# Optimization experiments

Measured on AMD Instinct MI355X. Metric: run time of the kernel, lower is better.

Reference implementation:

```python
import jax, jax.numpy as jnp
import numpy as np

N = 50000
NEG_SLOPE = 0.2


def add_self_loops(edge_index, n):
    loop = jnp.arange(n, dtype=edge_index.dtype)
    return jnp.concatenate([edge_index, jnp.stack([loop, loop])], axis=1)


def gatv2_conv(x, edge_index, Wl, bl, Wr, br, att, bias):
    """PyG GATv2Conv (share_weights=False, concat=True, add_self_loops applied by caller).
    x: [N, Fin]; edge_index: [2, E] with row0=src(j), row1=dst(i); att: [H, D].
    Returns (out [N, H*D], alpha [E, H])."""
    src, dst = edge_index[0], edge_index[1]
    H, D = att.shape
    n = x.shape[0]
    xl = (x @ Wl + bl).reshape(n, H, D)   # source-side transform
    xr = (x @ Wr + br).reshape(n, H, D)   # target-side transform
    e = jax.nn.leaky_relu(xl[src] + xr[dst], NEG_SLOPE)        # [E, H, D]
    logit = jnp.einsum('ehd,hd->eh', e, att)                    # [E, H]
    # segment softmax over edges grouped by target node
    lmax = jax.ops.segment_max(logit, dst, num_segments=n)      # [N, H]
    ex = jnp.exp(logit - lmax[dst])
    denom = jax.ops.segment_sum(ex, dst, num_segments=n)
    alpha = ex / denom[dst]                                     # [E, H]
    out = jax.ops.segment_sum(alpha[:, :, None] * xl[src], dst, num_segments=n)  # [N, H, D]
    return out.reshape(n, H * D) + bias, alpha


def setup_inputs() -> dict:
    key = jax.random.key(0)
    ks = jax.random.split(key, 16)
    E = 400000
    x = jax.random.normal(ks[0], (N, 23), dtype=jnp.float32)
    edge_index = jax.random.randint(ks[1], (2, E), 0, N, dtype=jnp.int64)
    H1, D1 = 8, 64
    F1 = H1 * D1  # 512
    s = 0.1
    return {
        'x': x,
        'edge_index': edge_index,
        'Wl1': jax.random.normal(ks[2], (23, F1), dtype=jnp.float32) * s,
        'bl1': jnp.zeros((F1,), jnp.float32),
        'Wr1': jax.random.normal(ks[3], (23, F1), dtype=jnp.float32) * s,
        'br1': jnp.zeros((F1,), jnp.float32),
        'att1': jax.random.normal(ks[4], (H1, D1), dtype=jnp.float32) * s,
        'bias1': jnp.zeros((F1,), jnp.float32),
        'Wl2': jax.random.normal(ks[5], (F1, 1), dtype=jnp.float32) * s,
        'bl2': jnp.zeros((1,), jnp.float32),
        'Wr2': jax.random.normal(ks[6], (F1, 1), dtype=jnp.float32) * s,
        'br2': jnp.zeros((1,), jnp.float32),
        'att2': jax.random.normal(ks[7], (1, 1), dtype=jnp.float32) * s,
        'bias2': jnp.zeros((1,), jnp.float32),
    }


def reference(x, edge_index, Wl1, bl1, Wr1, br1, att1, bias1,
              Wl2, bl2, Wr2, br2, att2, bias2):
    ei = add_self_loops(edge_index, N)
    h, _ = gatv2_conv(x, ei, Wl1, bl1, Wr1, br1, att1, bias1)
    h = jax.nn.relu(h)
    h, alpha = gatv2_conv(h, ei, Wl2, bl2, Wr2, br2, att2, bias2)
    return h, alpha
```

## Files before the change

### kernel.cpp

```cpp
#include <hip/hip_runtime.h>
#include <math.h>

#define NN 50000
#define E0 400000
#define EE 450000
#define FF 512
#define G1 2048
#define NPB 25
#define EPB 220
#define WAVES_TOTAL (G1 * 4)
#define MAXD 64
#define LOG2E 1.44269504f

typedef _Float16 h2 __attribute__((ext_vector_type(2)));

__device__ __forceinline__ h2 uas_h2(unsigned u) { union { unsigned u; h2 h; } c; c.u = u; return c.h; }
__device__ __forceinline__ unsigned h2as_u(h2 h) { union { unsigned u; h2 h; } c; c.h = h; return c.u; }
__device__ __forceinline__ unsigned packh(float a, float b) {
    h2 hh = { (_Float16)a, (_Float16)b };
    return h2as_u(hh);
}
__device__ __forceinline__ float leaky(float v) { return fmaxf(v, 0.2f * v); }

template <int CTRL>
__device__ __forceinline__ float dpp_add(float v) {
    int x = __builtin_bit_cast(int, v);
    int y = __builtin_amdgcn_update_dpp(0, x, CTRL, 0xF, 0xF, true);
    return v + __builtin_bit_cast(float, y);
}

__global__ __launch_bounds__(256) void k_predeg(
    const float* __restrict__ x,
    const float* __restrict__ Wl1, const float* __restrict__ bl1,
    const float* __restrict__ Wr1, const float* __restrict__ br1,
    const int* __restrict__ ei,
    unsigned* __restrict__ xlh, unsigned* __restrict__ xrh,
    int* __restrict__ cnt, int* __restrict__ src_sl)
{
    __shared__ unsigned sxh[NPB * 12];
    int b = blockIdx.x, t = threadIdx.x;

    {
        int e0 = b * EPB;
        int e1 = e0 + EPB; if (e1 > EE) e1 = EE;
        for (int e = e0 + t; e < e1; e += 256) {
            int src, dst;
            if (e < E0) { src = ei[e]; dst = ei[E0 + e]; }
            else        { src = e - E0; dst = src; }
            int p = atomicAdd(&cnt[dst], 1);
            if (p < MAXD) src_sl[(size_t)dst * MAXD + p] = src;
        }
    }

    int i0 = b * NPB;
    int i1 = i0 + NPB; if (i1 > NN) i1 = NN;
    int nnod = i1 - i0;
    for (int k = t; k < nnod * 12; k += 256) {
        int n = k / 12, j = k - n * 12;
        const float* row = x + (size_t)(i0 + n) * 23;
        float f0 = row[2 * j];
        float f1 = (2 * j + 1 < 23) ? row[2 * j + 1] : 0.f;
        sxh[n * 12 + j] = packh(f0, f1);
    }

    int c0 = 2 * t, c1 = 2 * t + 1;
    h2 wl0[12], wl1v[12], wr0[12], wr1v[12];
#pragma unroll
    for (int j = 0; j < 12; j++) {
        int r0 = 2 * j, r1 = 2 * j + 1;
        float a, b2;
        a = Wl1[r0 * FF + c0]; b2 = (r1 < 23) ? Wl1[r1 * FF + c0] : 0.f;
        wl0[j] = (h2){ (_Float16)a, (_Float16)b2 };
        a = Wl1[r0 * FF + c1]; b2 = (r1 < 23) ? Wl1[r1 * FF + c1] : 0.f;
        wl1v[j] = (h2){ (_Float16)a, (_Float16)b2 };
        a = Wr1[r0 * FF + c0]; b2 = (r1 < 23) ? Wr1[r1 * FF + c0] : 0.f;
        wr0[j] = (h2){ (_Float16)a, (_Float16)b2 };
        a = Wr1[r0 * FF + c1]; b2 = (r1 < 23) ? Wr1[r1 * FF + c1] : 0.f;
        wr1v[j] = (h2){ (_Float16)a, (_Float16)b2 };
    }
    float bl0 = bl1[c0], bl1s = bl1[c1];
    float br0 = br1[c0], br1s = br1[c1];
    __syncthreads();

    const uint4* S = (const uint4*)sxh;
    for (int n = 0; n < nnod; n++) {
        uint4 xa = S[n * 3 + 0];
        uint4 xb = S[n * 3 + 1];
        uint4 xc = S[n * 3 + 2];
        h2 xv[12] = { uas_h2(xa.x), uas_h2(xa.y), uas_h2(xa.z), uas_h2(xa.w),
                      uas_h2(xb.x), uas_h2(xb.y), uas_h2(xb.z), uas_h2(xb.w),
                      uas_h2(xc.x), uas_h2(xc.y), uas_h2(xc.z), uas_h2(xc.w) };
        float al0 = bl0, al1 = bl1s, ar0 = br0, ar1 = br1s;
#pragma unroll
        for (int j = 0; j < 12; j++) {
            al0 = __builtin_amdgcn_fdot2(wl0[j], xv[j], al0, false);
            al1 = __builtin_amdgcn_fdot2(wl1v[j], xv[j], al1, false);
            ar0 = __builtin_amdgcn_fdot2(wr0[j], xv[j], ar0, false);
            ar1 = __builtin_amdgcn_fdot2(wr1v[j], xv[j], ar1, false);
        }
        xlh[(size_t)(i0 + n) * 256 + t] = packh(al0, al1);
        xrh[(size_t)(i0 + n) * 256 + t] = packh(ar0, ar1);
    }
}

__global__ __launch_bounds__(256) void k_layer1(
    const uint4* __restrict__ xlh, const uint4* __restrict__ xrh,
    const float* __restrict__ att, const float* __restrict__ bias1,
    const float* __restrict__ Wl2, const float* __restrict__ bl2,
    const float* __restrict__ Wr2, const float* __restrict__ br2,
    const int* __restrict__ cnt, const int* __restrict__ src_sl,
    float* __restrict__ xl2, float* __restrict__ xr2)
{
    int t = threadIdx.x;
    int l = t & 63;
    int wid = blockIdx.x * 4 + (t >> 6);

    float4 atA = ((const float4*)att)[2 * l];
    float4 atB = ((const float4*)att)[2 * l + 1];
    h2 a6_0 = { (_Float16)(0.6f * LOG2E * atA.x), (_Float16)(0.6f * LOG2E * atA.y) };
    h2 a6_1 = { (_Float16)(0.6f * LOG2E * atA.z), (_Float16)(0.6f * LOG2E * atA.w) };
    h2 a6_2 = { (_Float16)(0.6f * LOG2E * atB.x), (_Float16)(0.6f * LOG2E * atB.y) };
    h2 a6_3 = { (_Float16)(0.6f * LOG2E * atB.z), (_Float16)(0.6f * LOG2E * atB.w) };
    h2 a4_0 = { (_Float16)(0.4f * LOG2E * atA.x), (_Float16)(0.4f * LOG2E * atA.y) };
    h2 a4_1 = { (_Float16)(0.4f * LOG2E * atA.z), (_Float16)(0.4f * LOG2E * atA.w) };
    h2 a4_2 = { (_Float16)(0.4f * LOG2E * atB.x), (_Float16)(0.4f * LOG2E * atB.y) };
    h2 a4_3 = { (_Float16)(0.4f * LOG2E * atB.z), (_Float16)(0.4f * LOG2E * atB.w) };
    float bl2v = bl2[0], br2v = br2[0];

    int i = wid;
    int dg0 = 0, myj = 0; uint4 xq = {0, 0, 0, 0};
    if (i < NN) {
        dg0 = cnt[i];
        myj = src_sl[(size_t)i * MAXD + l];
        xq  = xrh[(size_t)i * 64 + l];
    }

    for (; i < NN; i += WAVES_TOTAL) {
        int dg = dg0; if (dg > MAXD) dg = MAXD;

        int s0 = 0;
        int s1 = (dg > 1) ? 1 : 0;
        int s2 = (dg > 2) ? 2 : s1;
        int s3 = (dg > 3) ? 3 : s2;
        uint4 ra = xlh[(size_t)__builtin_amdgcn_readlane(myj, s0) * 64 + l];
        uint4 rb = xlh[(size_t)__builtin_amdgcn_readlane(myj, s1) * 64 + l];
        uint4 rc = xlh[(size_t)__builtin_amdgcn_readlane(myj, s2) * 64 + l];
        uint4 rd = xlh[(size_t)__builtin_amdgcn_readlane(myj, s3) * 64 + l];

        int inext = i + WAVES_TOTAL;
        int dg_n = 0, myj_n = 0; uint4 xq_n = {0, 0, 0, 0};
        if (inext < NN) {
            dg_n  = cnt[inext];
            myj_n = src_sl[(size_t)inext * MAXD + l];
            xq_n  = xrh[(size_t)inext * 64 + l];
        }

        h2 q0 = uas_h2(xq.x), q1 = uas_h2(xq.y), q2 = uas_h2(xq.z), q3 = uas_h2(xq.w);

        float s = 0.f;
        h2 A0 = { 0, 0 }, A1 = { 0, 0 }, A2 = { 0, 0 }, A3 = { 0, 0 };

#define PROC(RV)                                                               \
        {                                                                      \
            h2 p0 = uas_h2(RV.x), p1 = uas_h2(RV.y),                           \
               p2 = uas_h2(RV.z), p3 = uas_h2(RV.w);                           \
            h2 t0 = p0 + q0, t1 = p1 + q1, t2 = p2 + q2, t3 = p3 + q3;         \
            h2 b0 = uas_h2(h2as_u(t0) & 0x7fff7fffu);                          \
            h2 b1 = uas_h2(h2as_u(t1) & 0x7fff7fffu);                          \
            h2 b2 = uas_h2(h2as_u(t2) & 0x7fff7fffu);                          \
            h2 b3 = uas_h2(h2as_u(t3) & 0x7fff7fffu);                          \
            float part = 0.f;                                                  \
            part = __builtin_amdgcn_fdot2(a6_0, t0, part, false);              \
            part = __builtin_amdgcn_fdot2(a4_0, b0, part, false);              \
            part = __builtin_amdgcn_fdot2(a6_1, t1, part, false);              \
            part = __builtin_amdgcn_fdot2(a4_1, b1, part, false);              \
            part = __builtin_amdgcn_fdot2(a6_2, t2, part, false);              \
            part = __builtin_amdgcn_fdot2(a4_2, b2, part, false);              \
            part = __builtin_amdgcn_fdot2(a6_3, t3, part, false);              \
            part = __builtin_amdgcn_fdot2(a4_3, b3, part, false);              \
            part = dpp_add<0xB1>(part);                                        \
            part = dpp_add<0x4E>(part);                                        \
            part = dpp_add<0x141>(part);                                       \
            float wv = exp2f(part);                                            \
            s += wv;                                                           \
            _Float16 wh = (_Float16)wv;                                        \
            h2 w2 = { wh, wh };                                                \
            A0 += w2 * p0;                                                     \
            A1 += w2 * p1;                                                     \
            A2 += w2 * p2;                                                     \
            A3 += w2 * p3;                                                     \
        }

        int p = 0;
        for (;;) {
            PROC(ra);
            if (++p >= dg) break;
            { int sl = p + 3 < dg ? p + 3 : dg - 1;
              ra = xlh[(size_t)__builtin_amdgcn_readlane(myj, sl) * 64 + l]; }
            PROC(rb);
            if (++p >= dg) break;
            { int sl = p + 3 < dg ? p + 3 : dg - 1;
              rb = xlh[(size_t)__builtin_amdgcn_readlane(myj, sl) * 64 + l]; }
            PROC(rc);
            if (++p >= dg) break;
            { int sl = p + 3 < dg ? p + 3 : dg - 1;
              rc = xlh[(size_t)__builtin_amdgcn_readlane(myj, sl) * 64 + l]; }
            PROC(rd);
            if (++p >= dg) break;
            { int sl = p + 3 < dg ? p + 3 : dg - 1;
              rd = xlh[(size_t)__builtin_amdgcn_readlane(myj, sl) * 64 + l]; }
        }
#undef PROC

        float inv = 1.f / s;
        float4 bA = ((const float4*)bias1)[2 * l];
        float4 bB = ((const float4*)bias1)[2 * l + 1];
        float h0 = fmaxf(fmaf((float)A0[0], inv, bA.x), 0.f);
        float h1 = fmaxf(fmaf((float)A0[1], inv, bA.y), 0.f);
        float h2v = fmaxf(fmaf((float)A1[0], inv, bA.z), 0.f);
        float h3 = fmaxf(fmaf((float)A1[1], inv, bA.w), 0.f);
        float h4 = fmaxf(fmaf((float)A2[0], inv, bB.x), 0.f);
        float h5 = fmaxf(fmaf((float)A2[1], inv, bB.y), 0.f);
        float h6 = fmaxf(fmaf((float)A3[0], inv, bB.z), 0.f);
        float h7 = fmaxf(fmaf((float)A3[1], inv, bB.w), 0.f);

        float4 wlA = ((const float4*)Wl2)[2 * l];
        float4 wlB = ((const float4*)Wl2)[2 * l + 1];
        float4 wrA = ((const float4*)Wr2)[2 * l];
        float4 wrB = ((const float4*)Wr2)[2 * l + 1];
        float pl = h0 * wlA.x + h1 * wlA.y + h2v * wlA.z + h3 * wlA.w
                 + h4 * wlB.x + h5 * wlB.y + h6 * wlB.z + h7 * wlB.w;
        float pr = h0 * wrA.x + h1 * wrA.y + h2v * wrA.z + h3 * wrA.w
                 + h4 * wrB.x + h5 * wrB.y + h6 * wrB.z + h7 * wrB.w;
#pragma unroll
        for (int o = 32; o > 0; o >>= 1) {
            pl += __shfl_xor(pl, o, 64);
            pr += __shfl_xor(pr, o, 64);
        }
        if (l == 0) {
            xl2[i] = pl + bl2v;
            xr2[i] = pr + br2v;
        }

        dg0 = dg_n; myj = myj_n; xq = xq_n;
    }
}

__global__ void k_layer2a(const float* __restrict__ xl2, const float* __restrict__ xr2,
                          const float* __restrict__ att2, const float* __restrict__ bias2,
                          const int* __restrict__ cnt, const int* __restrict__ src_sl,
                          float* __restrict__ out, float* __restrict__ invs)
{
    int i = blockIdx.x * blockDim.x + threadIdx.x;
    if (i >= NN) return;
    int dg = cnt[i]; if (dg > MAXD) dg = MAXD;
    const int* sp = src_sl + (size_t)i * MAXD;
    float xri = xr2[i];
    float a2l = att2[0] * LOG2E;
    float s = 0.f, num = 0.f;
    for (int p = 0; p < dg; p++) {
        float v = xl2[sp[p]];
        float w = exp2f(leaky(v + xri) * a2l);
        s += w;
        num = fmaf(w, v, num);
    }
    out[i] = num / s + bias2[0];
    invs[i] = 1.f / s;
}

__global__ void k_layer2b(const float* __restrict__ xl2, const float* __restrict__ xr2,
                          const float* __restrict__ att2, const int* __restrict__ ei,
                          const float* __restrict__ invs, float* __restrict__ out)
{
    int e = blockIdx.x * blockDim.x + threadIdx.x;
    if (e >= EE) return;
    int src, dst;
    if (e < E0) { src = ei[e]; dst = ei[E0 + e]; }
    else        { src = e - E0; dst = src; }
    float a2l = att2[0] * LOG2E;
    float lg = leaky(xl2[src] + xr2[dst]) * a2l;
    out[NN + e] = exp2f(lg) * invs[dst];
}

extern "C" void kernel_launch(void* const* d_in, const int* in_sizes, int n_in,
                              void* d_out, int out_size, void* d_ws, size_t ws_size,
                              hipStream_t stream)
{
    const float* x     = (const float*)d_in[0];
    const int*   ei    = (const int*)d_in[1];
    const float* Wl1   = (const float*)d_in[2];
    const float* bl1   = (const float*)d_in[3];
    const float* Wr1   = (const float*)d_in[4];
    const float* br1   = (const float*)d_in[5];
    const float* att1  = (const float*)d_in[6];
    const float* bias1 = (const float*)d_in[7];
    const float* Wl2   = (const float*)d_in[8];
    const float* bl2   = (const float*)d_in[9];
    const float* Wr2   = (const float*)d_in[10];
    const float* br2   = (const float*)d_in[11];
    const float* att2  = (const float*)d_in[12];
    const float* bias2 = (const float*)d_in[13];
    float* out = (float*)d_out;

    char* ws = (char*)d_ws;
    unsigned* xlh  = (unsigned*)ws; ws += (size_t)NN * 256 * 4;
    unsigned* xrh  = (unsigned*)ws; ws += (size_t)NN * 256 * 4;
    float* xl2     = (float*)ws;    ws += (size_t)NN * 4;
    float* xr2     = (float*)ws;    ws += (size_t)NN * 4;
    float* invs    = (float*)ws;    ws += (size_t)NN * 4;
    int* cnt       = (int*)ws;      ws += (size_t)NN * 4;
    int* src_sl    = (int*)ws;      ws += (size_t)NN * MAXD * 4;

    (void)hipMemsetAsync(cnt, 0, (size_t)NN * 4, stream);

    k_predeg<<<G1, 256, 0, stream>>>(x, Wl1, bl1, Wr1, br1, ei, xlh, xrh,
                                     cnt, src_sl);
    k_layer1<<<G1, 256, 0, stream>>>((const uint4*)xlh, (const uint4*)xrh,
                                     att1, bias1, Wl2, bl2, Wr2, br2,
                                     cnt, src_sl, xl2, xr2);
    k_layer2a<<<(NN + 255) / 256, 256, 0, stream>>>(xl2, xr2, att2, bias2,
                                                    cnt, src_sl, out, invs);
    k_layer2b<<<(EE + 255) / 256, 256, 0, stream>>>(xl2, xr2, att2, ei, invs, out);
}
```

Baseline: 222.5 us.

## Process two destination nodes per wave with interleaved neighbor gathers

The fused layer-1 aggregation kernel now handles two target nodes per wavefront at once, interleaving their neighbor loads and softmax-weighted accumulation so that two independent gather chains are in flight. The prefetch depth per node drops from four to two slots, and the stride becomes twice the wave count. The aim is to hide gather latency with cross-node independence instead of deeper per-node prefetch. The cost is more registers and extra divergence when the two nodes have different degrees. The wid mapping assumes 2*WAVES_TOTAL covers the nodes, and the first loads are unguarded (cnt[iA] is read even if iA >= NN).

```diff
diff --git a/kernel.cpp b/kernel.cpp
--- a/kernel.cpp
+++ b/kernel.cpp
@@ -127,44 +127,51 @@
     h2 a4_3 = { (_Float16)(0.4f * LOG2E * atB.z), (_Float16)(0.4f * LOG2E * atB.w) };
     float bl2v = bl2[0], br2v = br2[0];
 
-    int i = wid;
-    int dg0 = 0, myj = 0; uint4 xq = {0, 0, 0, 0};
-    if (i < NN) {
-        dg0 = cnt[i];
-        myj = src_sl[(size_t)i * MAXD + l];
-        xq  = xrh[(size_t)i * 64 + l];
-    }
-
-    for (; i < NN; i += WAVES_TOTAL) {
-        int dg = dg0; if (dg > MAXD) dg = MAXD;
-
-        int s0 = 0;
-        int s1 = (dg > 1) ? 1 : 0;
-        int s2 = (dg > 2) ? 2 : s1;
-        int s3 = (dg > 3) ? 3 : s2;
-        uint4 ra = xlh[(size_t)__builtin_amdgcn_readlane(myj, s0) * 64 + l];
-        uint4 rb = xlh[(size_t)__builtin_amdgcn_readlane(myj, s1) * 64 + l];
-        uint4 rc = xlh[(size_t)__builtin_amdgcn_readlane(myj, s2) * 64 + l];
-        uint4 rd = xlh[(size_t)__builtin_amdgcn_readlane(myj, s3) * 64 + l];
-
-        int inext = i + WAVES_TOTAL;
-        int dg_n = 0, myj_n = 0; uint4 xq_n = {0, 0, 0, 0};
-        if (inext < NN) {
-            dg_n  = cnt[inext];
-            myj_n = src_sl[(size_t)inext * MAXD + l];
-            xq_n  = xrh[(size_t)inext * 64 + l];
-        }
-
-        h2 q0 = uas_h2(xq.x), q1 = uas_h2(xq.y), q2 = uas_h2(xq.z), q3 = uas_h2(xq.w);
-
-        float s = 0.f;
-        h2 A0 = { 0, 0 }, A1 = { 0, 0 }, A2 = { 0, 0 }, A3 = { 0, 0 };
-
-#define PROC(RV)                                                               \
+    int iA = 2 * wid, iB = iA + 1;
+    int dgA = cnt[iA];
+    int dgB = (iB < NN) ? cnt[iB] : 0;
+    int myjA = (l < dgA) ? src_sl[(size_t)iA * MAXD + l] : 0;
+    int myjB = (iB < NN && l < dgB) ? src_sl[(size_t)iB * MAXD + l] : 0;
+
+    while (iA < NN) {
+        if (dgA > MAXD) dgA = MAXD;
+        if (dgB > MAXD) dgB = MAXD;
+        bool hasB = (iB < NN);
+
+        uint4 xqA = xrh[(size_t)iA * 64 + l];
+        uint4 xqB = xqA;
+        if (hasB) xqB = xrh[(size_t)iB * 64 + l];
+
+        uint4 raA = xlh[(size_t)__builtin_amdgcn_readlane(myjA, 0) * 64 + l];
+        uint4 rbA = raA;
+        if (dgA > 1) rbA = xlh[(size_t)__builtin_amdgcn_readlane(myjA, 1) * 64 + l];
+        uint4 raB = raA, rbB = raA;
+        if (hasB) {
+            raB = xlh[(size_t)__builtin_amdgcn_readlane(myjB, 0) * 64 + l];
+            rbB = raB;
+            if (dgB > 1) rbB = xlh[(size_t)__builtin_amdgcn_readlane(myjB, 1) * 64 + l];
+        }
+
+        int iA_n = iA + 2 * WAVES_TOTAL, iB_n = iA_n + 1;
+        int dgA_n = 0, dgB_n = 0, myjA_n = 0, myjB_n = 0;
+        if (iA_n < NN) dgA_n = cnt[iA_n];
+        if (iB_n < NN) dgB_n = cnt[iB_n];
+        myjA_n = (iA_n < NN && l < dgA_n) ? src_sl[(size_t)iA_n * MAXD + l] : 0;
+        myjB_n = (iB_n < NN && l < dgB_n) ? src_sl[(size_t)iB_n * MAXD + l] : 0;
+
+        h2 qA0 = uas_h2(xqA.x), qA1 = uas_h2(xqA.y), qA2 = uas_h2(xqA.z), qA3 = uas_h2(xqA.w);
+        h2 qB0 = uas_h2(xqB.x), qB1 = uas_h2(xqB.y), qB2 = uas_h2(xqB.z), qB3 = uas_h2(xqB.w);
+
+        float sA = 0.f, sB = 0.f;
+        h2 accA0 = {0,0}, accA1 = {0,0}, accA2 = {0,0}, accA3 = {0,0};
+        h2 accB0 = {0,0}, accB1 = {0,0}, accB2 = {0,0}, accB3 = {0,0};
+
+#define PROC(N, RV)                                                            \
         {                                                                      \
             h2 p0 = uas_h2(RV.x), p1 = uas_h2(RV.y),                           \
                p2 = uas_h2(RV.z), p3 = uas_h2(RV.w);                           \
-            h2 t0 = p0 + q0, t1 = p1 + q1, t2 = p2 + q2, t3 = p3 + q3;         \
+            h2 t0 = p0 + q##N##0, t1 = p1 + q##N##1,                           \
+               t2 = p2 + q##N##2, t3 = p3 + q##N##3;                           \
             h2 b0 = uas_h2(h2as_u(t0) & 0x7fff7fffu);                          \
             h2 b1 = uas_h2(h2as_u(t1) & 0x7fff7fffu);                          \
             h2 b2 = uas_h2(h2as_u(t2) & 0x7fff7fffu);                          \
@@ -182,67 +189,83 @@
             part = dpp_add<0x4E>(part);                                        \
             part = dpp_add<0x141>(part);                                       \
             float wv = exp2f(part);                                            \
-            s += wv;                                                           \
+            s##N += wv;                                                        \
             _Float16 wh = (_Float16)wv;                                        \
             h2 w2 = { wh, wh };                                                \
-            A0 += w2 * p0;                                                     \
-            A1 += w2 * p1;                                                     \
-            A2 += w2 * p2;                                                     \
-            A3 += w2 * p3;                                                     \
-        }
-
+            acc##N##0 += w2 * p0;                                              \
+            acc##N##1 += w2 * p1;                                              \
+            acc##N##2 += w2 * p2;                                              \
+            acc##N##3 += w2 * p3;                                              \
+        }
+
+        int m = dgA > dgB ? dgA : dgB;
         int p = 0;
         for (;;) {
-            PROC(ra);
-            if (++p >= dg) break;
-            { int sl = p + 3 < dg ? p + 3 : dg - 1;
-              ra = xlh[(size_t)__builtin_amdgcn_readlane(myj, sl) * 64 + l]; }
-            PROC(rb);
-            if (++p >= dg) break;
-            { int sl = p + 3 < dg ? p + 3 : dg - 1;
-              rb = xlh[(size_t)__builtin_amdgcn_readlane(myj, sl) * 64 + l]; }
-            PROC(rc);
-            if (++p >= dg) break;
-            { int sl = p + 3 < dg ? p + 3 : dg - 1;
-              rc = xlh[(size_t)__builtin_amdgcn_readlane(myj, sl) * 64 + l]; }
-            PROC(rd);
-            if (++p >= dg) break;
-            { int sl = p + 3 < dg ? p + 3 : dg - 1;
-              rd = xlh[(size_t)__builtin_amdgcn_readlane(myj, sl) * 64 + l]; }
+            if (p < dgA) {
+                PROC(A, raA);
+                if (p + 2 < dgA)
+                    raA = xlh[(size_t)__builtin_amdgcn_readlane(myjA, p + 2) * 64 + l];
+            }
+            if (p < dgB) {
+                PROC(B, raB);
+                if (p + 2 < dgB)
+                    raB = xlh[(size_t)__builtin_amdgcn_readlane(myjB, p + 2) * 64 + l];
+            }
+            if (++p >= m) break;
+            if (p < dgA) {
+                PROC(A, rbA);
+                if (p + 2 < dgA)
+                    rbA = xlh[(size_t)__builtin_amdgcn_readlane(myjA, p + 2) * 64 + l];
+            }
+            if (p < dgB) {
+                PROC(B, rbB);
+                if (p + 2 < dgB)
+                    rbB = xlh[(size_t)__builtin_amdgcn_readlane(myjB, p + 2) * 64 + l];
+            }
+            if (++p >= m) break;
         }
 #undef PROC
 
-        float inv = 1.f / s;
         float4 bA = ((const float4*)bias1)[2 * l];
         float4 bB = ((const float4*)bias1)[2 * l + 1];
-        float h0 = fmaxf(fmaf((float)A0[0], inv, bA.x), 0.f);
-        float h1 = fmaxf(fmaf((float)A0[1], inv, bA.y), 0.f);
-        float h2v = fmaxf(fmaf((float)A1[0], inv, bA.z), 0.f);
-        float h3 = fmaxf(fmaf((float)A1[1], inv, bA.w), 0.f);
-        float h4 = fmaxf(fmaf((float)A2[0], inv, bB.x), 0.f);
-        float h5 = fmaxf(fmaf((float)A2[1], inv, bB.y), 0.f);
-        float h6 = fmaxf(fmaf((float)A3[0], inv, bB.z), 0.f);
-        float h7 = fmaxf(fmaf((float)A3[1], inv, bB.w), 0.f);
-
         float4 wlA = ((const float4*)Wl2)[2 * l];
         float4 wlB = ((const float4*)Wl2)[2 * l + 1];
         float4 wrA = ((const float4*)Wr2)[2 * l];
         float4 wrB = ((const float4*)Wr2)[2 * l + 1];
-        float pl = h0 * wlA.x + h1 * wlA.y + h2v * wlA.z + h3 * wlA.w
-                 + h4 * wlB.x + h5 * wlB.y + h6 * wlB.z + h7 * wlB.w;
-        float pr = h0 * wrA.x + h1 * wrA.y + h2v * wrA.z + h3 * wrA.w
-                 + h4 * wrB.x + h5 * wrB.y + h6 * wrB.z + h7 * wrB.w;
-#pragma unroll
-        for (int o = 32; o > 0; o >>= 1) {
-            pl += __shfl_xor(pl, o, 64);
-            pr += __shfl_xor(pr, o, 64);
-        }
-        if (l == 0) {
-            xl2[i] = pl + bl2v;
-            xr2[i] = pr + br2v;
-        }
-
-        dg0 = dg_n; myj = myj_n; xq = xq_n;
+
+#define EPILOG(N, ii)                                                          \
+        {                                                                      \
+            float inv = 1.f / s##N;                                            \
+            float h0 = fmaxf(fmaf((float)acc##N##0[0], inv, bA.x), 0.f);       \
+            float h1 = fmaxf(fmaf((float)acc##N##0[1], inv, bA.y), 0.f);       \
+            float h2v = fmaxf(fmaf((float)acc##N##1[0], inv, bA.z), 0.f);      \
+            float h3 = fmaxf(fmaf((float)acc##N##1[1], inv, bA.w), 0.f);       \
+            float h4 = fmaxf(fmaf((float)acc##N##2[0], inv, bB.x), 0.f);       \
+            float h5 = fmaxf(fmaf((float)acc##N##2[1], inv, bB.y), 0.f);       \
+            float h6 = fmaxf(fmaf((float)acc##N##3[0], inv, bB.z), 0.f);       \
+            float h7 = fmaxf(fmaf((float)acc##N##3[1], inv, bB.w), 0.f);       \
+            float pl = h0 * wlA.x + h1 * wlA.y + h2v * wlA.z + h3 * wlA.w      \
+                     + h4 * wlB.x + h5 * wlB.y + h6 * wlB.z + h7 * wlB.w;      \
+            float pr = h0 * wrA.x + h1 * wrA.y + h2v * wrA.z + h3 * wrA.w      \
+                     + h4 * wrB.x + h5 * wrB.y + h6 * wrB.z + h7 * wrB.w;      \
+            _Pragma("unroll")                                                  \
+            for (int o = 32; o > 0; o >>= 1) {                                 \
+                pl += __shfl_xor(pl, o, 64);                                   \
+                pr += __shfl_xor(pr, o, 64);                                   \
+            }                                                                  \
+            if (l == 0) {                                                      \
+                xl2[ii] = pl + bl2v;                                           \
+                xr2[ii] = pr + br2v;                                           \
+            }                                                                  \
+        }
+
+        EPILOG(A, iA);
+        if (hasB) EPILOG(B, iB);
+#undef EPILOG
+
+        iA = iA_n; iB = iB_n;
+        dgA = dgA_n; dgB = dgB_n;
+        myjA = myjA_n; myjB = myjB_n;
     }
 }
 
```

New measurement: 231.2 us. 1.04x slower.
